# Kernel optimization log

Hardware: AMD Instinct MI355X
Metric: run time of the kernel (lower is better)

Reference implementation:

```python
import jax, jax.numpy as jnp
import numpy as np

H = 8  # number of heads


def setup_inputs() -> dict:
    key = jax.random.key(0)
    ks = jax.random.split(key, 7)
    B, L, D = 4, 2048, 512
    dh = D // H
    s = 1.0 / np.sqrt(D).astype(np.float32)
    return {
        "q": jax.random.normal(ks[0], (B, L, D), jnp.float32),
        "k": jax.random.normal(ks[1], (B, L, D), jnp.float32),
        "v": jax.random.normal(ks[2], (B, L, D), jnp.float32),
        "Wq": jax.random.normal(ks[3], (D, D), jnp.float32) * s,
        "Wk": jax.random.normal(ks[4], (D, D), jnp.float32) * s,
        "Wv": jax.random.normal(ks[5], (D, D), jnp.float32) * s,
        "E": jax.random.normal(ks[6], (L, dh), jnp.float32) * s,
    }


def _skew(QE):
    # QE: [B, H, L, L] -> pad one column on the left, reshape to [B,H,L+1,L],
    # drop the first row: the classic Music Transformer skewing trick.
    B, h, L, M = QE.shape
    padded = jnp.pad(QE, ((0, 0), (0, 0), (0, 0), (1, 0)))
    return padded.reshape(B, h, M + 1, L)[:, :, 1:, :]


def reference(q, k, v, Wq, Wk, Wv, E):
    B, L, D = q.shape
    dh = D // H

    def heads(x, W):
        return jnp.einsum('bld,de->ble', x, W).reshape(B, L, H, dh).transpose(0, 2, 1, 3)

    qh = heads(q, Wq)  # [B,H,L,dh]
    kh = heads(k, Wk)
    vh = heads(v, Wv)

    QE = jnp.einsum('bhld,md->bhlm', qh, E)      # [B,H,L,L]
    Srel = _skew(QE)                             # [B,H,L,L]
    QKt = jnp.einsum('bhld,bhmd->bhlm', qh, kh)  # [B,H,L,L]

    # NOTE: original divides AFTER softmax (faithful to source).
    attn = jax.nn.softmax(QKt + Srel, axis=-1) / float(np.sqrt(dh))
    out = jnp.einsum('bhlm,bhmd->bhld', attn, vh)
    return out.transpose(0, 2, 1, 3).reshape(B, L, D)
```

## Files before the change

### kernel.cpp

```cpp
#include <hip/hip_runtime.h>
#include <hip/hip_bf16.h>
#include <math.h>

typedef _Float16 f16;
typedef __attribute__((ext_vector_type(8))) _Float16 f16x8;
typedef __attribute__((ext_vector_type(4))) _Float16 f16x4;
typedef __attribute__((ext_vector_type(4))) float f32x4;

namespace {
constexpr int B = 4, L = 2048, D = 512, NH = 8, DH = 64;
}

__global__ __launch_bounds__(256)
void ecast_kernel(const float* __restrict__ E, f16* __restrict__ Ef) {
    int i4 = (blockIdx.x * 256 + threadIdx.x) * 4;
    float4 x = *(const float4*)(E + i4);
    *(f16x4*)(Ef + i4) = (f16x4){(f16)x.x, (f16)x.y, (f16)x.z, (f16)x.w};
}

__global__ __launch_bounds__(256)
void wtrans_kernel(const float* __restrict__ Wq, const float* __restrict__ Wk,
                   const float* __restrict__ Wv, f16* __restrict__ Wt) {
    __shared__ f16 Ws[64 * 65];
    const int sel = blockIdx.z;
    const float* W = (sel == 0) ? Wq : (sel == 1) ? Wk : Wv;
    f16* Wo = Wt + (size_t)sel * D * D;
    const int k0 = blockIdx.x * 64, n0 = blockIdx.y * 64;
    const int t = threadIdx.x;
#pragma unroll
    for (int i = 0; i < 16; ++i) {
        int idx = 256 * i + t;
        int r = idx >> 6, c = idx & 63;
        Ws[r * 65 + c] = (f16)W[(size_t)(k0 + r) * D + n0 + c];
    }
    __syncthreads();
    const int c = t >> 2, kseg = t & 3;
    f16x8 r0, r1;
#pragma unroll
    for (int j = 0; j < 8; ++j) r0[j] = Ws[(kseg * 16 + j) * 65 + c];
#pragma unroll
    for (int j = 0; j < 8; ++j) r1[j] = Ws[(kseg * 16 + 8 + j) * 65 + c];
    f16* o = Wo + (size_t)(n0 + c) * D + k0 + kseg * 16;
    *(f16x8*)o = r0;
    *(f16x8*)(o + 8) = r1;
}

__global__ __launch_bounds__(256, 4)
void proj_gemm(const float* __restrict__ q, const float* __restrict__ k,
               const float* __restrict__ v, const f16* __restrict__ Wt,
               f16* __restrict__ Qf, f16* __restrict__ Kf, f16* __restrict__ Vtf) {
    __shared__ f16 As[128 * 72];
    __shared__ f16 Bs[64 * 72];
    const int bx = blockIdx.x, by = blockIdx.y;
    const int sel = by >> 3, h = by & 7;
    const int m0 = bx * 128;
    const float* X = (sel == 0) ? q : (sel == 1) ? k : v;
    const f16* Bt = Wt + (size_t)sel * D * D + (size_t)h * 64 * D;
    const int t = threadIdx.x, wid = t >> 6, lane = t & 63;
    const int quad = lane >> 4, col = lane & 15;
    const int mw = wid * 32;

    f32x4 acc[2][4];
#pragma unroll
    for (int i = 0; i < 2; ++i)
#pragma unroll
        for (int j = 0; j < 4; ++j) acc[i][j] = (f32x4){0.f, 0.f, 0.f, 0.f};

    float4 xa[8];
    f16x8 breg[2];
    auto loadG = [&](int k0) {
#pragma unroll
        for (int i = 0; i < 8; ++i) {
            int idx = 256 * i + t;
            int r = idx >> 4, c4 = idx & 15;
            xa[i] = *(const float4*)(X + (size_t)(m0 + r) * D + k0 + c4 * 4);
        }
#pragma unroll
        for (int i = 0; i < 2; ++i) {
            int idx = 256 * i + t;
            int r = idx >> 3, ch = idx & 7;
            breg[i] = *(const f16x8*)(Bt + (size_t)r * D + k0 + ch * 8);
        }
    };
    auto storeL = [&]() {
#pragma unroll
        for (int i = 0; i < 8; ++i) {
            int idx = 256 * i + t;
            int r = idx >> 4, c4 = idx & 15;
            *(f16x4*)(As + r * 72 + c4 * 4) =
                (f16x4){(f16)xa[i].x, (f16)xa[i].y, (f16)xa[i].z, (f16)xa[i].w};
        }
#pragma unroll
        for (int i = 0; i < 2; ++i) {
            int idx = 256 * i + t;
            int r = idx >> 3, ch = idx & 7;
            *(f16x8*)(Bs + r * 72 + ch * 8) = breg[i];
        }
    };

    loadG(0);
    for (int k0 = 0; k0 < D; k0 += 64) {
        __syncthreads();
        storeL();
        __syncthreads();
        if (k0 + 64 < D) loadG(k0 + 64);
#pragma unroll
        for (int ks = 0; ks < 2; ++ks) {
            f16x8 af[2], bf[4];
#pragma unroll
            for (int mt = 0; mt < 2; ++mt)
                af[mt] = *(const f16x8*)(As + (mw + mt * 16 + col) * 72 + quad * 8 + ks * 32);
#pragma unroll
            for (int nt = 0; nt < 4; ++nt)
                bf[nt] = *(const f16x8*)(Bs + (nt * 16 + col) * 72 + quad * 8 + ks * 32);
#pragma unroll
            for (int mt = 0; mt < 2; ++mt)
#pragma unroll
                for (int nt = 0; nt < 4; ++nt)
                    acc[mt][nt] = __builtin_amdgcn_mfma_f32_16x16x32_f16(af[mt], bf[nt], acc[mt][nt], 0, 0, 0);
        }
    }

    if (sel < 2) {
        f16* Y = (sel == 0) ? Qf : Kf;
#pragma unroll
        for (int mt = 0; mt < 2; ++mt)
#pragma unroll
            for (int nt = 0; nt < 4; ++nt)
#pragma unroll
                for (int reg = 0; reg < 4; ++reg) {
                    int m = m0 + mw + mt * 16 + quad * 4 + reg;
                    int bb = m >> 11, l = m & 2047, d = nt * 16 + col;
                    Y[((size_t)(bb * NH + h) * L + l) * DH + d] = (f16)acc[mt][nt][reg];
                }
    } else {
        __syncthreads();
        f16* Cs = As;
#pragma unroll
        for (int mt = 0; mt < 2; ++mt)
#pragma unroll
            for (int nt = 0; nt < 4; ++nt)
#pragma unroll
                for (int reg = 0; reg < 4; ++reg) {
                    int d = nt * 16 + col;
                    int lc = mw + mt * 16 + quad * 4 + reg;
                    Cs[d * 136 + lc] = (f16)acc[mt][nt][reg];
                }
        __syncthreads();
        const int dd = t >> 2, seg = t & 3;
        const int bb = m0 >> 11, l0 = m0 & 2047;
        f16* Yv = Vtf + ((size_t)(bb * NH + h) * DH + dd) * L + l0 + seg * 32;
#pragma unroll
        for (int j = 0; j < 4; ++j)
            *(f16x8*)(Yv + j * 8) = *(const f16x8*)(Cs + dd * 136 + seg * 32 + j * 8);
    }
}

__global__ __launch_bounds__(256, 4)
void attn_kernel(const f16* __restrict__ Qf, const f16* __restrict__ Kf,
                 const f16* __restrict__ Vtf, const f16* __restrict__ Ef,
                 float* __restrict__ out) {
    __shared__ f16 KfS[64 * 72];
    __shared__ f16 VfS[64 * 72];
    __shared__ f16 Pbuf[4][16 * 72];

    const int t = threadIdx.x, wid = t >> 6, lane = t & 63;
    const int quad = lane >> 4, col = lane & 15;
    const int l0w = blockIdx.x * 64 + wid * 16;
    const int h = blockIdx.y, bb = blockIdx.z;
    const size_t head = (size_t)(bb * NH + h) * (size_t)(L * DH);
    const f16* qf = Qf + head;
    const f16* kf = Kf + head;
    const f16* vt = Vtf + head;
    f16* Pw = Pbuf[wid];

    f16x8 qF[2], qS[2];
    {
        const int m = l0w + col;
        const int mS = min(m + 1, L - 1);
#pragma unroll
        for (int ks = 0; ks < 2; ++ks) {
            const int off = quad * 8 + ks * 32;
            qF[ks] = *(const f16x8*)(qf + (size_t)m * DH + off);
            qS[ks] = *(const f16x8*)(qf + (size_t)mS * DH + off);
        }
    }

    f16x8 kreg[2], vreg[2];
    auto loadKV = [&](int c0) {
#pragma unroll
        for (int i = 0; i < 2; ++i) {
            int idx = 256 * i + t;
            int r = idx >> 3, ch = idx & 7;
            kreg[i] = *(const f16x8*)(kf + (size_t)(c0 + r) * DH + ch * 8);
            vreg[i] = *(const f16x8*)(vt + (size_t)r * L + c0 + ch * 8);
        }
    };

    f32x4 O[4];
#pragma unroll
    for (int i = 0; i < 4; ++i) O[i] = (f32x4){0.f, 0.f, 0.f, 0.f};
    float mrow[4] = {-1e30f, -1e30f, -1e30f, -1e30f};
    float srow[4] = {0.f, 0.f, 0.f, 0.f};

    loadKV(0);
    for (int c0 = 0; c0 < L; c0 += 64) {
        __syncthreads();
#pragma unroll
        for (int i = 0; i < 2; ++i) {
            int idx = 256 * i + t;
            int r = idx >> 3, ch = idx & 7;
            *(f16x8*)(KfS + r * 72 + ch * 8) = kreg[i];
            *(f16x8*)(VfS + r * 72 + ch * 8) = vreg[i];
        }
        __syncthreads();
        if (c0 + 64 < L) loadKV(c0 + 64);

        const int d0 = c0 - l0w;

        f32x4 S[4];
#pragma unroll
        for (int ns = 0; ns < 4; ++ns) {
            S[ns] = (f32x4){0.f, 0.f, 0.f, 0.f};
#pragma unroll
            for (int ks = 0; ks < 2; ++ks) {
                f16x8 bh = *(const f16x8*)(KfS + (ns * 16 + col) * 72 + quad * 8 + ks * 32);
                S[ns] = __builtin_amdgcn_mfma_f32_16x16x32_f16(qF[ks], bh, S[ns], 0, 0, 0);
            }
        }

        const bool doA = (d0 <= 15);
        const bool doB = (d0 >= -61);
#pragma unroll 1
        for (int pass = 0; pass < 2; ++pass) {
            if ((pass == 0 && !doA) || (pass == 1 && !doB)) continue;
            const int jbase = (pass == 0) ? (d0 + L - 16) : (d0 - 17);
            f32x4 G[5];
#pragma unroll
            for (int g = 0; g < 5; ++g) {
                int er = min(max(jbase + g * 16 + col, 0), L - 1);
                G[g] = (f32x4){0.f, 0.f, 0.f, 0.f};
                const size_t eb = (size_t)er * DH + quad * 8;
#pragma unroll
                for (int ks = 0; ks < 2; ++ks) {
                    f16x8 e8 = *(const f16x8*)(Ef + eb + ks * 32);
                    G[g] = __builtin_amdgcn_mfma_f32_16x16x32_f16(
                               (pass == 0) ? qF[ks] : qS[ks], e8, G[g], 0, 0, 0);
                }
            }
#pragma unroll
            for (int reg = 0; reg < 4; ++reg) {
                const int r  = quad * 4 + reg;
                const int jj = col - r + 15;
                const int src = quad * 16 + (jj & 15);
#pragma unroll
                for (int ns = 0; ns < 4; ++ns) {
                    float v0 = __shfl(G[ns][reg], src, 64);
                    float v1 = __shfl(G[ns + 1][reg], src, 64);
                    float val = (jj < 16) ? v0 : v1;
                    const int rel = d0 + ns * 16 + col - r;
                    const bool use = (pass == 0) ? (rel <= 0) : (rel >= 2);
                    if (use) S[ns][reg] += val;
                }
            }
        }

#pragma unroll
        for (int reg = 0; reg < 4; ++reg) {
            float tm = fmaxf(fmaxf(S[0][reg], S[1][reg]), fmaxf(S[2][reg], S[3][reg]));
#pragma unroll
            for (int msk = 1; msk < 16; msk <<= 1)
                tm = fmaxf(tm, __shfl_xor(tm, msk, 16));
            const float mnew  = fmaxf(mrow[reg], tm);
            const float alpha = __expf(mrow[reg] - mnew);
            float p[4], ps = 0.f;
#pragma unroll
            for (int ns = 0; ns < 4; ++ns) { p[ns] = __expf(S[ns][reg] - mnew); ps += p[ns]; }
#pragma unroll
            for (int msk = 1; msk < 16; msk <<= 1)
                ps += __shfl_xor(ps, msk, 16);
            srow[reg] = srow[reg] * alpha + ps;
            mrow[reg] = mnew;
            const int r = quad * 4 + reg;
#pragma unroll
            for (int ns = 0; ns < 4; ++ns) {
                O[ns][reg] *= alpha;
                Pw[r * 72 + ns * 16 + col] = (f16)p[ns];
            }
        }

        f16x8 pA[2];
        pA[0] = *(const f16x8*)(Pw + col * 72 + quad * 8);
        pA[1] = *(const f16x8*)(Pw + col * 72 + 32 + quad * 8);
#pragma unroll
        for (int ns = 0; ns < 4; ++ns) {
#pragma unroll
            for (int ks = 0; ks < 2; ++ks) {
                f16x8 v8 = *(const f16x8*)(VfS + (ns * 16 + col) * 72 + quad * 8 + ks * 32);
                O[ns] = __builtin_amdgcn_mfma_f32_16x16x32_f16(pA[ks], v8, O[ns], 0, 0, 0);
            }
        }
    }

#pragma unroll
    for (int reg = 0; reg < 4; ++reg) {
        const int l = l0w + quad * 4 + reg;
        const float inv = 1.0f / (srow[reg] * 8.0f);
        float* o = out + ((size_t)bb * L + l) * D + h * DH;
#pragma unroll
        for (int ns = 0; ns < 4; ++ns)
            o[ns * 16 + col] = O[ns][reg] * inv;
    }
}

extern "C" void kernel_launch(void* const* d_in, const int* in_sizes, int n_in,
                              void* d_out, int out_size, void* d_ws, size_t ws_size,
                              hipStream_t stream) {
    const float* q  = (const float*)d_in[0];
    const float* k  = (const float*)d_in[1];
    const float* v  = (const float*)d_in[2];
    const float* Wq = (const float*)d_in[3];
    const float* Wk = (const float*)d_in[4];
    const float* Wv = (const float*)d_in[5];
    const float* E  = (const float*)d_in[6];
    float* out = (float*)d_out;

    const size_t plane = (size_t)B * NH * L * DH;
    f16* Qf  = (f16*)d_ws;
    f16* Kfp = Qf + plane;
    f16* Vtf = Kfp + plane;
    f16* Wt  = Vtf + plane;
    f16* Ef  = Wt + (size_t)3 * D * D;

    ecast_kernel<<<L * DH / 1024, 256, 0, stream>>>(E, Ef);
    wtrans_kernel<<<dim3(8, 8, 3), 256, 0, stream>>>(Wq, Wk, Wv, Wt);
    proj_gemm<<<dim3(64, 24), 256, 0, stream>>>(q, k, v, Wt, Qf, Kfp, Vtf);
    attn_kernel<<<dim3(L / 64, NH, B), 256, 0, stream>>>(Qf, Kfp, Vtf, Ef, out);
}
```

Baseline: 352.6 us.

## Split attention KV range in two halves with combine kernel and double-buffered LDS

Splits the key/value sequence of each attention block into two halves, doubling the grid. Each half writes unnormalized f16 partial outputs with per-row max and sum, and a new combine kernel merges them into the final fp32 output. K/V shared tiles are double-buffered so one barrier per iteration is removed. The split adds partial-result traffic and an extra launch, and rounds partial outputs to f16. Dropping the occupancy hint in launch_bounds and doubling LDS may also lower occupancy.

```diff
diff --git a/kernel.cpp b/kernel.cpp
--- a/kernel.cpp
+++ b/kernel.cpp
@@ -9,6 +9,7 @@
 
 namespace {
 constexpr int B = 4, L = 2048, D = 512, NH = 8, DH = 64;
+constexpr int HALF = 1024;
 }
 
 __global__ __launch_bounds__(256)
@@ -156,18 +157,21 @@
     }
 }
 
-__global__ __launch_bounds__(256, 4)
+__global__ __launch_bounds__(256)
 void attn_kernel(const f16* __restrict__ Qf, const f16* __restrict__ Kf,
                  const f16* __restrict__ Vtf, const f16* __restrict__ Ef,
-                 float* __restrict__ out) {
-    __shared__ f16 KfS[64 * 72];
-    __shared__ f16 VfS[64 * 72];
+                 f16* __restrict__ Opart, float* __restrict__ Mpart,
+                 float* __restrict__ Spart) {
+    __shared__ f16 KS[2][64 * 72];
+    __shared__ f16 VS[2][64 * 72];
     __shared__ f16 Pbuf[4][16 * 72];
 
     const int t = threadIdx.x, wid = t >> 6, lane = t & 63;
     const int quad = lane >> 4, col = lane & 15;
     const int l0w = blockIdx.x * 64 + wid * 16;
-    const int h = blockIdx.y, bb = blockIdx.z;
+    const int h = blockIdx.y;
+    const int bb = blockIdx.z >> 1, half = blockIdx.z & 1;
+    const int c0beg = half * HALF, c0end = c0beg + HALF;
     const size_t head = (size_t)(bb * NH + h) * (size_t)(L * DH);
     const f16* qf = Qf + head;
     const f16* kf = Kf + head;
@@ -203,18 +207,20 @@
     float mrow[4] = {-1e30f, -1e30f, -1e30f, -1e30f};
     float srow[4] = {0.f, 0.f, 0.f, 0.f};
 
-    loadKV(0);
-    for (int c0 = 0; c0 < L; c0 += 64) {
-        __syncthreads();
+    loadKV(c0beg);
+    int buf = 0;
+    for (int c0 = c0beg; c0 < c0end; c0 += 64, buf ^= 1) {
+        f16* KSb = KS[buf];
+        f16* VSb = VS[buf];
 #pragma unroll
         for (int i = 0; i < 2; ++i) {
             int idx = 256 * i + t;
             int r = idx >> 3, ch = idx & 7;
-            *(f16x8*)(KfS + r * 72 + ch * 8) = kreg[i];
-            *(f16x8*)(VfS + r * 72 + ch * 8) = vreg[i];
-        }
-        __syncthreads();
-        if (c0 + 64 < L) loadKV(c0 + 64);
+            *(f16x8*)(KSb + r * 72 + ch * 8) = kreg[i];
+            *(f16x8*)(VSb + r * 72 + ch * 8) = vreg[i];
+        }
+        __syncthreads();
+        if (c0 + 64 < c0end) loadKV(c0 + 64);
 
         const int d0 = c0 - l0w;
 
@@ -224,7 +230,7 @@
             S[ns] = (f32x4){0.f, 0.f, 0.f, 0.f};
 #pragma unroll
             for (int ks = 0; ks < 2; ++ks) {
-                f16x8 bh = *(const f16x8*)(KfS + (ns * 16 + col) * 72 + quad * 8 + ks * 32);
+                f16x8 bh = *(const f16x8*)(KSb + (ns * 16 + col) * 72 + quad * 8 + ks * 32);
                 S[ns] = __builtin_amdgcn_mfma_f32_16x16x32_f16(qF[ks], bh, S[ns], 0, 0, 0);
             }
         }
@@ -296,7 +302,7 @@
         for (int ns = 0; ns < 4; ++ns) {
 #pragma unroll
             for (int ks = 0; ks < 2; ++ks) {
-                f16x8 v8 = *(const f16x8*)(VfS + (ns * 16 + col) * 72 + quad * 8 + ks * 32);
+                f16x8 v8 = *(const f16x8*)(VSb + (ns * 16 + col) * 72 + quad * 8 + ks * 32);
                 O[ns] = __builtin_amdgcn_mfma_f32_16x16x32_f16(pA[ks], v8, O[ns], 0, 0, 0);
             }
         }
@@ -305,12 +311,50 @@
 #pragma unroll
     for (int reg = 0; reg < 4; ++reg) {
         const int l = l0w + quad * 4 + reg;
-        const float inv = 1.0f / (srow[reg] * 8.0f);
-        float* o = out + ((size_t)bb * L + l) * D + h * DH;
+        const size_t row = ((size_t)(half * B + bb) * NH + h) * L + l;
+        f16* o = Opart + row * DH;
 #pragma unroll
         for (int ns = 0; ns < 4; ++ns)
-            o[ns * 16 + col] = O[ns][reg] * inv;
-    }
+            o[ns * 16 + col] = (f16)O[ns][reg];
+        if (col == 0) {
+            Mpart[row] = mrow[reg];
+            Spart[row] = srow[reg];
+        }
+    }
+}
+
+__global__ __launch_bounds__(256)
+void combine_kernel(const f16* __restrict__ Opart, const float* __restrict__ Mpart,
+                    const float* __restrict__ Spart, float* __restrict__ out) {
+    const int gid = blockIdx.x * 256 + threadIdx.x;
+    const int row = gid >> 3;
+    const int dseg = (gid & 7) * 8;
+    const int bb = row >> 14;
+    const int rem = row & 16383;
+    const int h = rem >> 11, l = rem & 2047;
+    const int HSTRIDE = B * NH * L;
+
+    const float m0 = Mpart[row], m1 = Mpart[row + HSTRIDE];
+    const float s0 = Spart[row], s1 = Spart[row + HSTRIDE];
+    const float m = fmaxf(m0, m1);
+    const float e0 = __expf(m0 - m), e1 = __expf(m1 - m);
+    const float inv = 1.0f / ((s0 * e0 + s1 * e1) * 8.0f);
+    const float w0 = e0 * inv, w1 = e1 * inv;
+
+    f16x8 o0 = *(const f16x8*)(Opart + (size_t)row * DH + dseg);
+    f16x8 o1 = *(const f16x8*)(Opart + ((size_t)row + HSTRIDE) * DH + dseg);
+    float* o = out + ((size_t)bb * L + l) * D + h * DH + dseg;
+    float4 lo, hi;
+    lo.x = (float)o0[0] * w0 + (float)o1[0] * w1;
+    lo.y = (float)o0[1] * w0 + (float)o1[1] * w1;
+    lo.z = (float)o0[2] * w0 + (float)o1[2] * w1;
+    lo.w = (float)o0[3] * w0 + (float)o1[3] * w1;
+    hi.x = (float)o0[4] * w0 + (float)o1[4] * w1;
+    hi.y = (float)o0[5] * w0 + (float)o1[5] * w1;
+    hi.z = (float)o0[6] * w0 + (float)o1[6] * w1;
+    hi.w = (float)o0[7] * w0 + (float)o1[7] * w1;
+    *(float4*)o = lo;
+    *(float4*)(o + 4) = hi;
 }
 
 extern "C" void kernel_launch(void* const* d_in, const int* in_sizes, int n_in,
@@ -331,9 +375,14 @@
     f16* Vtf = Kfp + plane;
     f16* Wt  = Vtf + plane;
     f16* Ef  = Wt + (size_t)3 * D * D;
+    f16* Opart = Ef + (size_t)L * DH;
+    float* Mpart = (float*)(Opart + 2 * plane);
+    float* Spart = Mpart + (size_t)2 * B * NH * L;
 
     ecast_kernel<<<L * DH / 1024, 256, 0, stream>>>(E, Ef);
     wtrans_kernel<<<dim3(8, 8, 3), 256, 0, stream>>>(Wq, Wk, Wv, Wt);
     proj_gemm<<<dim3(64, 24), 256, 0, stream>>>(q, k, v, Wt, Qf, Kfp, Vtf);
-    attn_kernel<<<dim3(L / 64, NH, B), 256, 0, stream>>>(Qf, Kfp, Vtf, Ef, out);
-}
+    attn_kernel<<<dim3(L / 64, NH, B * 2), 256, 0, stream>>>(Qf, Kfp, Vtf, Ef,
+                                                             Opart, Mpart, Spart);
+    combine_kernel<<<(B * NH * L * DH / 8) / 256, 256, 0, stream>>>(Opart, Mpart, Spart, out);
+}
```

After: 399.3 us. 13.3% more time.
